# Performance work log

Hardware: AMD Instinct MI355X
Metric: run time of the kernel (lower is better)

## Reference

```python
import jax, jax.numpy as jnp
import numpy as np

WH, WW = 8, 8          # window height/width
NH = 8                 # num heads
DIM = 256              # channels
B_ = 512               # num_windows * batch
N = WH * WW            # tokens per window
HD = DIM // NH         # head dim


def _rel_constants():
    # log-spaced continuous relative coords table (Swin-V2 CPB input)
    ch = np.arange(-(WH - 1), WH, dtype=np.float32) / (WH - 1)
    cw = np.arange(-(WW - 1), WW, dtype=np.float32) / (WW - 1)
    table = np.stack(np.meshgrid(ch, cw, indexing='ij'), axis=-1)[None] * 8.0  # [1,2WH-1,2WW-1,2]
    table = np.sign(table) * np.log2(np.abs(table) + 1.0) / np.log2(8.0)
    # relative position index
    coords = np.stack(np.meshgrid(np.arange(WH), np.arange(WW), indexing='ij'))
    cf = coords.reshape(2, -1)
    rel = (cf[:, :, None] - cf[:, None, :]).transpose(1, 2, 0).astype(np.int64)
    rel[..., 0] += WH - 1
    rel[..., 1] += WW - 1
    rel[..., 0] *= 2 * WW - 1
    idx = rel.sum(-1)  # [N,N]
    return jnp.asarray(table, dtype=jnp.float32), jnp.asarray(idx)

TABLE, IDX = _rel_constants()


def setup_inputs() -> dict:
    key = jax.random.key(0)
    ks = jax.random.split(key, 16)
    s = lambda k, shape, sc=0.02: (jax.random.normal(k, shape, dtype=jnp.float32) * sc)
    inp = {
        'x1': jax.random.normal(ks[0], (B_, N, DIM), dtype=jnp.float32),
        'x2': jax.random.normal(ks[1], (B_, N, DIM), dtype=jnp.float32),
        'qkv_w1': s(ks[2], (3 * DIM, DIM)),
        'q_bias_1': jnp.zeros((DIM,), jnp.float32),
        'v_bias_1': jnp.zeros((DIM,), jnp.float32),
        'proj_w1': s(ks[3], (DIM, DIM)),
        'proj_b1': jnp.zeros((DIM,), jnp.float32),
        'logit_scale_1': jnp.log(10.0) * jnp.ones((NH, 1, 1), jnp.float32),
        'cpb1_w1': s(ks[4], (512, 2), 0.1),
        'cpb1_b1': jnp.zeros((512,), jnp.float32),
        'cpb1_w2': s(ks[5], (NH, 512), 0.1),
        'pc1_w': s(ks[6], (NH, 2 * NH), 0.1),
        'pc1_b': jnp.zeros((NH,), jnp.float32),
        'qkv_w2': s(ks[7], (3 * DIM, DIM)),
        'q_bias_2': jnp.zeros((DIM,), jnp.float32),
        'v_bias_2': jnp.zeros((DIM,), jnp.float32),
        'proj_w2': s(ks[8], (DIM, DIM)),
        'proj_b2': jnp.zeros((DIM,), jnp.float32),
        'logit_scale_2': jnp.log(10.0) * jnp.ones((NH, 1, 1), jnp.float32),
        'cpb2_w1': s(ks[9], (512, 2), 0.1),
        'cpb2_b1': jnp.zeros((512,), jnp.float32),
        'cpb2_w2': s(ks[10], (NH, 512), 0.1),
        'pc2_w': s(ks[11], (NH, 2 * NH), 0.1),
        'pc2_b': jnp.zeros((NH,), jnp.float32),
    }
    return inp


def _qkv(x, w, qb, vb):
    b = jnp.concatenate([qb, jnp.zeros_like(vb), vb])
    y = (x @ w.T + b).reshape(x.shape[0], N, 3, NH, HD).transpose(2, 0, 3, 1, 4)
    return y[0], y[1], y[2]  # each [B_, NH, N, HD]


def _l2norm(t):
    n = jnp.linalg.norm(t, axis=-1, keepdims=True)
    return t / jnp.maximum(n, 1e-12)


def _view(qn, k_same_n, k_diff_n, v, logit_scale, pc_w, pc_b, cw1, cb1, cw2, proj_w, proj_b):
    same = jnp.einsum('bhnd,bhmd->bhnm', qn, k_same_n)
    diff = jnp.einsum('bhnd,bhmd->bhnm', qn, k_diff_n)
    cat = jnp.concatenate([same, diff], axis=1).transpose(0, 2, 3, 1)  # [B,N,N,2H]
    scale = jnp.exp(jnp.minimum(logit_scale, jnp.log(100.0)))  # clamp at 1/0.01
    attn = (cat @ pc_w.T + pc_b).transpose(0, 3, 1, 2) * scale  # [B,H,N,N]
    # CPB MLP -> bias table -> gather
    tbl = (jax.nn.relu(TABLE @ cw1.T + cb1) @ cw2.T).reshape(-1, NH)  # [(2WH-1)*(2WW-1), H]
    bias = tbl[IDX.reshape(-1)].reshape(N, N, NH).transpose(2, 0, 1)  # [H,N,N]
    attn = attn + (16.0 * jax.nn.sigmoid(bias))[None]
    attn = jax.nn.softmax(attn, axis=-1)
    out = jnp.einsum('bhnm,bhmd->bhnd', attn, v).transpose(0, 2, 1, 3).reshape(-1, N, DIM)
    return out @ proj_w.T + proj_b


def reference(x1, x2, qkv_w1, q_bias_1, v_bias_1, proj_w1, proj_b1, logit_scale_1,
              cpb1_w1, cpb1_b1, cpb1_w2, pc1_w, pc1_b,
              qkv_w2, q_bias_2, v_bias_2, proj_w2, proj_b2, logit_scale_2,
              cpb2_w1, cpb2_b1, cpb2_w2, pc2_w, pc2_b):
    q1, k1, v1 = _qkv(x1, qkv_w1, q_bias_1, v_bias_1)
    q2, k2, v2 = _qkv(x2, qkv_w2, q_bias_2, v_bias_2)
    q1n, k1n = _l2norm(q1), _l2norm(k1)
    q2n, k2n = _l2norm(q2), _l2norm(k2)
    o1 = _view(q1n, k1n, k2n, v1, logit_scale_1, pc1_w, pc1_b, cpb1_w1, cpb1_b1, cpb1_w2, proj_w1, proj_b1)
    o2 = _view(q2n, k2n, k1n, v2, logit_scale_2, pc2_w, pc2_b, cpb2_w1, cpb2_b1, cpb2_w2, proj_w2, proj_b2)
    return o1, o2
```

## Files before the change

### kernel.cpp

```cpp
#include <hip/hip_runtime.h>

typedef _Float16 f16;
typedef f16  f16x8  __attribute__((ext_vector_type(8)));
typedef f16  f16x4v __attribute__((ext_vector_type(4)));
typedef f16  f16x2  __attribute__((ext_vector_type(2)));
typedef float f32x4 __attribute__((ext_vector_type(4)));

#define MFMA_F16(a,b,c) __builtin_amdgcn_mfma_f32_16x16x32_f16((a),(b),(c),0,0,0)

#define NWIN 512
#define SB_QST 3088
#define SB_KST 48
#define BUFX_ST 264
#define BUFO_HEAD 2304
#define VT_ST 72
#define SM_BYTES 70656
#define STBL_OFF 49408

__device__ __forceinline__ f16x8 ld_f16x8(const float* __restrict__ p) {
  f32x4 a = *(const f32x4*)p;
  f32x4 b = *(const f32x4*)(p + 4);
  f16x8 r;
  r[0] = (f16)a[0]; r[1] = (f16)a[1]; r[2] = (f16)a[2]; r[3] = (f16)a[3];
  r[4] = (f16)b[0]; r[5] = (f16)b[1]; r[6] = (f16)b[2]; r[7] = (f16)b[3];
  return r;
}

__global__ __launch_bounds__(256) void prep_all(
    const float* __restrict__ w1a, const float* __restrict__ b1a,
    const float* __restrict__ w2a,
    const float* __restrict__ w1b, const float* __restrict__ b1b,
    const float* __restrict__ w2b,
    const float* __restrict__ qkvw1, const float* __restrict__ qkvw2,
    const float* __restrict__ pw1, const float* __restrict__ pw2,
    float* __restrict__ sg16,
    f16* __restrict__ wq1f, f16* __restrict__ wq2f,
    f16* __restrict__ pw1f, f16* __restrict__ pw2f) {
  const int b = blockIdx.x;
  if (b >= 450) {
    const int cb = b - 450;
    const float* src; f16* dst; int base;
    if (cb < 96)       { src = qkvw1; dst = wq1f; base = cb * 2048; }
    else if (cb < 192) { src = qkvw2; dst = wq2f; base = (cb - 96) * 2048; }
    else if (cb < 224) { src = pw1;   dst = pw1f; base = (cb - 192) * 2048; }
    else               { src = pw2;   dst = pw2f; base = (cb - 224) * 2048; }
    const int o = base + threadIdx.x * 8;
    *(f16x8*)(dst + o) = ld_f16x8(src + o);
    return;
  }
  const int view = b / 225;
  const int e    = b % 225;
  const float* __restrict__ w1 = view ? w1b : w1a;
  const float* __restrict__ b1 = view ? b1b : b1a;
  const float* __restrict__ w2 = view ? w2b : w2a;
  const int t = threadIdx.x;
  const int i = e / 15, j = e % 15;
  const float vi = 8.0f * (float)(i - 7) * (1.0f / 7.0f);
  const float vj = 8.0f * (float)(j - 7) * (1.0f / 7.0f);
  const float in0 = copysignf(log2f(fabsf(vi) + 1.0f) * (1.0f / 3.0f), vi);
  const float in1 = copysignf(log2f(fabsf(vj) + 1.0f) * (1.0f / 3.0f), vj);
  float acc[8] = {0.f,0.f,0.f,0.f,0.f,0.f,0.f,0.f};
#pragma unroll
  for (int uu = 0; uu < 2; ++uu) {
    const int u = t + uu * 256;
    float hv = fmaxf(w1[2*u] * in0 + w1[2*u+1] * in1 + b1[u], 0.0f);
#pragma unroll
    for (int hh = 0; hh < 8; ++hh) acc[hh] += w2[hh*512 + u] * hv;
  }
#pragma unroll
  for (int off = 32; off >= 1; off >>= 1)
#pragma unroll
    for (int hh = 0; hh < 8; ++hh) acc[hh] += __shfl_xor(acc[hh], off, 64);
  __shared__ float red[4][8];
  if ((t & 63) == 0) {
#pragma unroll
    for (int hh = 0; hh < 8; ++hh) red[t >> 6][hh] = acc[hh];
  }
  __syncthreads();
  if (t < 8) {
    float s = red[0][t] + red[1][t] + red[2][t] + red[3][t];
    sg16[(view * 225 + e) * 8 + t] = 16.0f / (1.0f + __expf(-s));
  }
}

__global__ __launch_bounds__(512, 2) void fused_attn(
    const float* __restrict__ x1, const float* __restrict__ x2,
    const f16* __restrict__ qkvw1, const float* __restrict__ qb1, const float* __restrict__ vb1,
    const f16* __restrict__ qkvw2, const float* __restrict__ qb2, const float* __restrict__ vb2,
    const float* __restrict__ pcw1, const float* __restrict__ pcb1, const float* __restrict__ ls1,
    const float* __restrict__ pcw2, const float* __restrict__ pcb2, const float* __restrict__ ls2,
    const f16* __restrict__ pw1, const float* __restrict__ pb1,
    const f16* __restrict__ pw2, const float* __restrict__ pb2,
    const float* __restrict__ sg16,
    float* __restrict__ outp) {
  const int win = blockIdx.x;
  const int tid = threadIdx.x;
  const int lane = tid & 63, h = tid >> 6;
  const int quad = lane >> 4, m = lane & 15;

  __shared__ __align__(16) char sm[SM_BYTES];
  f16* bufX  = (f16*)sm;
  f16* bufO  = (f16*)(sm + 33792);
  char* Sbc  = sm;
  f16* preB  = (f16*)sm;
  float* sTbl = (float*)(sm + STBL_OFF);

  const f32x4 z4 = {0.f, 0.f, 0.f, 0.f};
  f16x8 aqF[2][4], kfF[2][4], bvF[2][2][2];
  f16* oh = bufO + h * BUFO_HEAD;

  for (int view = 0; view < 2; ++view) {
    const float* __restrict__ xv = (view ? x2 : x1) + (size_t)win * (64 * 256);
    const f16* __restrict__ W    = view ? qkvw2 : qkvw1;
    const float* __restrict__ qb = view ? qb2 : qb1;
    const float* __restrict__ vb = view ? vb2 : vb1;

    __syncthreads();
    for (int i = tid; i < 2048; i += 512) {
      const int row = i >> 5, c8 = i & 31;
      *(f16x8*)(bufX + row * BUFX_ST + c8 * 8) = ld_f16x8(xv + row * 256 + c8 * 8);
    }
    __syncthreads();

    for (int sec = 0; sec < 3; ++sec) {
      f32x4 acc0[4], acc1[4];
#pragma unroll
      for (int t = 0; t < 4; ++t) { acc0[t] = z4; acc1[t] = z4; }
      const f16* wb = W + (size_t)(sec * 256 + h * 32) * 256 + quad * 8;
#pragma unroll 2
      for (int k8 = 0; k8 < 8; ++k8) {
        f16x8 a0 = *(const f16x8*)(wb + (size_t)m * 256 + k8 * 32);
        f16x8 a1 = *(const f16x8*)(wb + (size_t)(16 + m) * 256 + k8 * 32);
#pragma unroll
        for (int tt = 0; tt < 4; ++tt) {
          f16x8 bfr = *(const f16x8*)(bufX + (tt * 16 + m) * BUFX_ST + k8 * 32 + quad * 8);
          acc0[tt] = MFMA_F16(a0, bfr, acc0[tt]);
          acc1[tt] = MFMA_F16(a1, bfr, acc1[tt]);
        }
      }
      float bs0[4], bs1[4];
#pragma unroll
      for (int r = 0; r < 4; ++r) {
        int c0 = h * 32 + quad * 4 + r;
        bs0[r] = (sec == 0) ? qb[c0] : (sec == 2 ? vb[c0] : 0.f);
        bs1[r] = (sec == 0) ? qb[c0 + 16] : (sec == 2 ? vb[c0 + 16] : 0.f);
      }
#pragma unroll
      for (int tt = 0; tt < 4; ++tt) {
        float v0[4], v1[4];
#pragma unroll
        for (int r = 0; r < 4; ++r) { v0[r] = acc0[tt][r] + bs0[r]; v1[r] = acc1[tt][r] + bs1[r]; }
        if (sec < 2) {
          float ss = 0.f;
#pragma unroll
          for (int r = 0; r < 4; ++r) ss += v0[r] * v0[r] + v1[r] * v1[r];
          ss += __shfl_xor(ss, 16, 64);
          ss += __shfl_xor(ss, 32, 64);
          float s = 1.0f / fmaxf(sqrtf(ss), 1e-12f);
#pragma unroll
          for (int r = 0; r < 4; ++r) { v0[r] *= s; v1[r] *= s; }
        }
        const int n = tt * 16 + m;
        if (sec < 2) {
          f16x4v p0, p1;
#pragma unroll
          for (int r = 0; r < 4; ++r) { p0[r] = (f16)v0[r]; p1[r] = (f16)v1[r]; }
          char* ob = (char*)oh;
          const int sw = (n & 7) << 4;
          *(f16x4v*)(ob + ((n * 64 + quad * 8) ^ sw))      = p0;
          *(f16x4v*)(ob + ((n * 64 + 32 + quad * 8) ^ sw)) = p1;
        } else {
#pragma unroll
          for (int r = 0; r < 4; ++r) {
            oh[(quad * 4 + r) * VT_ST + n]      = (f16)v0[r];
            oh[(quad * 4 + 16 + r) * VT_ST + n] = (f16)v1[r];
          }
        }
      }
      if (sec == 0) {
#pragma unroll
        for (int rt = 0; rt < 4; ++rt) {
          const int n = rt * 16 + m;
          aqF[view][rt] = *(const f16x8*)((char*)oh + ((n * 64 + quad * 16) ^ ((n & 7) << 4)));
        }
      } else if (sec == 1) {
#pragma unroll
        for (int ct = 0; ct < 4; ++ct) {
          const int n = ct * 16 + m;
          kfF[view][ct] = *(const f16x8*)((char*)oh + ((n * 64 + quad * 16) ^ ((n & 7) << 4)));
        }
      } else {
#pragma unroll
        for (int nt = 0; nt < 2; ++nt)
#pragma unroll
          for (int kv = 0; kv < 2; ++kv)
            bvF[view][nt][kv] = *(const f16x8*)(oh + (nt * 16 + m) * VT_ST + kv * 32 + quad * 8);
      }
    }
  }
  __syncthreads();

  for (int i = tid; i < 3600; i += 512) sTbl[i] = sg16[i];

#pragma unroll
  for (int view = 0; view < 2; ++view) {
    const float* __restrict__ pcw = view ? pcw2 : pcw1;
    float pcwf[16];
#pragma unroll
    for (int c = 0; c < 16; ++c) pcwf[c] = pcw[h * 16 + c];
    const float pcb_h = (view ? pcb2 : pcb1)[h];
    const float lsv = (view ? ls2 : ls1)[h];
    const float scale_h = __expf(fminf(lsv, 4.6051702f));
    const float pcbs = pcb_h * scale_h;
    const float* tblv = sTbl + view * 1800;

    f32x4 oacc[4][2];
#pragma unroll
    for (int rt = 0; rt < 4; ++rt) {
      f16x8 aq = aqF[view][rt];
      __builtin_amdgcn_s_setprio(1);
#pragma unroll
      for (int ct = 0; ct < 4; ++ct) {
        const int kk = ct * 16 + m;
        const int wbase = kk * SB_KST + (h << 2);
        f32x4 Ss = MFMA_F16(aq, kfF[view][ct], z4);
        f32x4 Sd = MFMA_F16(aq, kfF[1 - view][ct], z4);
#pragma unroll
        for (int r = 0; r < 4; ++r) {
          f16x2 pr; pr[0] = (f16)Ss[r]; pr[1] = (f16)Sd[r];
          *(f16x2*)(Sbc + (quad * 4 + r) * SB_QST + wbase) = pr;
        }
      }
      __builtin_amdgcn_s_setprio(0);
      __syncthreads();

      const int n = rt * 16 + m;
      const int nh_ = n >> 3, nw_ = n & 7;
      const int rbase = m * SB_QST;
      float logit[16];
#pragma unroll
      for (int j = 0; j < 16; ++j) {
        const int mm = (j < 8) ? (quad * 8 + j) : (32 + quad * 8 + (j - 8));
        const int b0 = rbase + mm * SB_KST;
        f16x8 s0 = *(const f16x8*)(Sbc + b0);
        f16x8 s1 = *(const f16x8*)(Sbc + b0 + 16);
        float mix = 0.f;
#pragma unroll
        for (int c = 0; c < 4; ++c) {
          mix += pcwf[c]      * (float)s0[2*c] + pcwf[8 + c]  * (float)s0[2*c+1];
          mix += pcwf[4 + c]  * (float)s1[2*c] + pcwf[12 + c] * (float)s1[2*c+1];
        }
        const int idx = (nh_ - (mm >> 3) + 7) * 15 + (nw_ - (mm & 7) + 7);
        logit[j] = mix * scale_h + pcbs + tblv[idx * 8 + h];
      }
      float mx = -1e30f;
#pragma unroll
      for (int j = 0; j < 16; ++j) mx = fmaxf(mx, logit[j]);
      mx = fmaxf(mx, __shfl_xor(mx, 16, 64));
      mx = fmaxf(mx, __shfl_xor(mx, 32, 64));
      float p[16], sum = 0.f;
#pragma unroll
      for (int j = 0; j < 16; ++j) { p[j] = __expf(logit[j] - mx); sum += p[j]; }
      sum += __shfl_xor(sum, 16, 64);
      sum += __shfl_xor(sum, 32, 64);
      float inv = 1.0f / sum;
      f16x8 av0, av1;
#pragma unroll
      for (int j = 0; j < 8; ++j) { av0[j] = (f16)(p[j] * inv); av1[j] = (f16)(p[8 + j] * inv); }
      __builtin_amdgcn_s_setprio(1);
#pragma unroll
      for (int nt = 0; nt < 2; ++nt) {
        f32x4 z = z4;
        z = MFMA_F16(av0, bvF[view][nt][0], z);
        z = MFMA_F16(av1, bvF[view][nt][1], z);
        oacc[rt][nt] = z;
      }
      __builtin_amdgcn_s_setprio(0);
      __syncthreads();
    }

#pragma unroll
    for (int mt = 0; mt < 4; ++mt)
#pragma unroll
      for (int nt = 0; nt < 2; ++nt)
#pragma unroll
        for (int r = 0; r < 4; ++r)
          preB[(mt * 16 + quad * 4 + r) * 264 + h * 32 + nt * 16 + m] = (f16)oacc[mt][nt][r];
    __syncthreads();

    const f16* __restrict__ Wp = view ? pw2 : pw1;
    const float* __restrict__ pb = view ? pb2 : pb1;
    f32x4 pacc0[4], pacc1[4];
#pragma unroll
    for (int t = 0; t < 4; ++t) { pacc0[t] = z4; pacc1[t] = z4; }
#pragma unroll 2
    for (int ks = 0; ks < 8; ++ks) {
      f16x8 pa0 = *(const f16x8*)(Wp + (size_t)(h * 32 + m) * 256 + ks * 32 + quad * 8);
      f16x8 pa1 = *(const f16x8*)(Wp + (size_t)(h * 32 + 16 + m) * 256 + ks * 32 + quad * 8);
#pragma unroll
      for (int tt = 0; tt < 4; ++tt) {
        f16x8 bfr = *(const f16x8*)(preB + (tt * 16 + m) * 264 + ks * 32 + quad * 8);
        pacc0[tt] = MFMA_F16(pa0, bfr, pacc0[tt]);
        pacc1[tt] = MFMA_F16(pa1, bfr, pacc1[tt]);
      }
    }
    float* obase = outp + (size_t)(view * NWIN + win) * (64 * 256);
#pragma unroll
    for (int tt = 0; tt < 4; ++tt) {
      f32x4 p0, p1;
#pragma unroll
      for (int r = 0; r < 4; ++r) {
        p0[r] = pacc0[tt][r] + pb[h * 32 + quad * 4 + r];
        p1[r] = pacc1[tt][r] + pb[h * 32 + 16 + quad * 4 + r];
      }
      const int n = tt * 16 + m;
      *(f32x4*)(obase + n * 256 + h * 32 + quad * 4)      = p0;
      *(f32x4*)(obase + n * 256 + h * 32 + 16 + quad * 4) = p1;
    }
    __syncthreads();
  }
}

extern "C" void kernel_launch(void* const* d_in, const int* in_sizes, int n_in,
                              void* d_out, int out_size, void* d_ws, size_t ws_size,
                              hipStream_t stream) {
  (void)in_sizes; (void)n_in; (void)out_size; (void)ws_size;
  const float* x1   = (const float*)d_in[0];
  const float* x2   = (const float*)d_in[1];
  const float* qkvw1= (const float*)d_in[2];
  const float* qb1  = (const float*)d_in[3];
  const float* vb1  = (const float*)d_in[4];
  const float* pw1  = (const float*)d_in[5];
  const float* pb1  = (const float*)d_in[6];
  const float* ls1  = (const float*)d_in[7];
  const float* cw11 = (const float*)d_in[8];
  const float* cb11 = (const float*)d_in[9];
  const float* cw12 = (const float*)d_in[10];
  const float* pcw1 = (const float*)d_in[11];
  const float* pcb1 = (const float*)d_in[12];
  const float* qkvw2= (const float*)d_in[13];
  const float* qb2  = (const float*)d_in[14];
  const float* vb2  = (const float*)d_in[15];
  const float* pw2  = (const float*)d_in[16];
  const float* pb2  = (const float*)d_in[17];
  const float* ls2  = (const float*)d_in[18];
  const float* cw21 = (const float*)d_in[19];
  const float* cb21 = (const float*)d_in[20];
  const float* cw22 = (const float*)d_in[21];
  const float* pcw2 = (const float*)d_in[22];
  const float* pcb2 = (const float*)d_in[23];

  float* SG16 = (float*)d_ws;
  f16* wq1f = (f16*)((char*)d_ws + 14400);
  f16* wq2f = wq1f + 196608;
  f16* pw1f = wq2f + 196608;
  f16* pw2f = pw1f + 65536;
  float* out = (float*)d_out;

  prep_all<<<706, 256, 0, stream>>>(cw11, cb11, cw12, cw21, cb21, cw22,
                                    qkvw1, qkvw2, pw1, pw2,
                                    SG16, wq1f, wq2f, pw1f, pw2f);
  fused_attn<<<NWIN, 512, 0, stream>>>(x1, x2,
      wq1f, qb1, vb1, wq2f, qb2, vb2,
      pcw1, pcb1, ls1, pcw2, pcb2, ls2,
      pw1f, pb1, pw2f, pb2, SG16, out);
}
```

Measured before the change: 293.0 us.

## Fold head-mixing into K blend and process both views concurrently per block

```diff
diff --git a/kernel.cpp b/kernel.cpp
--- a/kernel.cpp
+++ b/kernel.cpp
@@ -3,19 +3,24 @@
 typedef _Float16 f16;
 typedef f16  f16x8  __attribute__((ext_vector_type(8)));
 typedef f16  f16x4v __attribute__((ext_vector_type(4)));
-typedef f16  f16x2  __attribute__((ext_vector_type(2)));
 typedef float f32x4 __attribute__((ext_vector_type(4)));
 
 #define MFMA_F16(a,b,c) __builtin_amdgcn_mfma_f32_16x16x32_f16((a),(b),(c),0,0,0)
 
 #define NWIN 512
-#define SB_QST 3088
-#define SB_KST 48
-#define BUFX_ST 264
-#define BUFO_HEAD 2304
-#define VT_ST 72
-#define SM_BYTES 70656
-#define STBL_OFF 49408
+#define RA 0
+#define RB 32768
+#define RC 65536
+#define RD 98304
+#define RE 131072
+#define SM_BYTES 163840
+
+__device__ __forceinline__ int swz512(int row, int colByte) {
+  return row * 512 + (colByte ^ ((row & 7) << 4));
+}
+__device__ __forceinline__ int swz128(int row, int colByte) {
+  return row * 128 + (colByte ^ ((row & 7) << 4));
+}
 
 __device__ __forceinline__ f16x8 ld_f16x8(const float* __restrict__ p) {
   f32x4 a = *(const f32x4*)p;
@@ -33,7 +38,7 @@
     const float* __restrict__ w2b,
     const float* __restrict__ qkvw1, const float* __restrict__ qkvw2,
     const float* __restrict__ pw1, const float* __restrict__ pw2,
-    float* __restrict__ sg16,
+    float* __restrict__ tblT,
     f16* __restrict__ wq1f, f16* __restrict__ wq2f,
     f16* __restrict__ pw1f, f16* __restrict__ pw2f) {
   const int b = blockIdx.x;
@@ -79,11 +84,11 @@
   __syncthreads();
   if (t < 8) {
     float s = red[0][t] + red[1][t] + red[2][t] + red[3][t];
-    sg16[(view * 225 + e) * 8 + t] = 16.0f / (1.0f + __expf(-s));
-  }
-}
-
-__global__ __launch_bounds__(512, 2) void fused_attn(
+    tblT[(view * 8 + t) * 226 + e] = 16.0f / (1.0f + __expf(-s));
+  }
+}
+
+__global__ __launch_bounds__(1024, 4) void fused_attn(
     const float* __restrict__ x1, const float* __restrict__ x2,
     const f16* __restrict__ qkvw1, const float* __restrict__ qb1, const float* __restrict__ vb1,
     const f16* __restrict__ qkvw2, const float* __restrict__ qb2, const float* __restrict__ vb2,
@@ -91,53 +96,57 @@
     const float* __restrict__ pcw2, const float* __restrict__ pcb2, const float* __restrict__ ls2,
     const f16* __restrict__ pw1, const float* __restrict__ pb1,
     const f16* __restrict__ pw2, const float* __restrict__ pb2,
-    const float* __restrict__ sg16,
+    const float* __restrict__ tblT,
     float* __restrict__ outp) {
-  const int win = blockIdx.x;
   const int tid = threadIdx.x;
-  const int lane = tid & 63, h = tid >> 6;
+  const int lane = tid & 63;
+  const int w = tid >> 6;
   const int quad = lane >> 4, m = lane & 15;
+  const int vgrp = w >> 3;
+  const int h = w & 7;
 
   __shared__ __align__(16) char sm[SM_BYTES];
-  f16* bufX  = (f16*)sm;
-  f16* bufO  = (f16*)(sm + 33792);
-  char* Sbc  = sm;
-  f16* preB  = (f16*)sm;
-  float* sTbl = (float*)(sm + STBL_OFF);
-
   const f32x4 z4 = {0.f, 0.f, 0.f, 0.f};
-  f16x8 aqF[2][4], kfF[2][4], bvF[2][2][2];
-  f16* oh = bufO + h * BUFO_HEAD;
-
-  for (int view = 0; view < 2; ++view) {
-    const float* __restrict__ xv = (view ? x2 : x1) + (size_t)win * (64 * 256);
-    const f16* __restrict__ W    = view ? qkvw2 : qkvw1;
-    const float* __restrict__ qb = view ? qb2 : qb1;
-    const float* __restrict__ vb = view ? vb2 : vb1;
-
-    __syncthreads();
-    for (int i = tid; i < 2048; i += 512) {
-      const int row = i >> 5, c8 = i & 31;
-      *(f16x8*)(bufX + row * BUFX_ST + c8 * 8) = ld_f16x8(xv + row * 256 + c8 * 8);
+
+  f16x8 bvF[2][2][2];
+
+  char* bufX = sm + (vgrp ? RB : RA);
+  char* Karr = sm + (vgrp ? RD : RC);
+  const f16* W = vgrp ? qkvw2 : qkvw1;
+  const float* qb = vgrp ? qb2 : qb1;
+  const float* vb = vgrp ? vb2 : vb1;
+
+  for (int wi = 0; wi < 2; ++wi) {
+    const int win = blockIdx.x * 2 + wi;
+
+    for (int i = tid; i < 4096; i += 1024) {
+      const int vv = i >> 11, row = (i >> 5) & 63, c8 = i & 31;
+      const float* src = (vv ? x2 : x1) + (size_t)win * (64 * 256) + row * 256 + c8 * 8;
+      *(f16x8*)(sm + (vv ? RB : RA) + swz512(row, c8 * 16)) = ld_f16x8(src);
     }
     __syncthreads();
 
-    for (int sec = 0; sec < 3; ++sec) {
+    for (int si = 0; si < 3; ++si) {
+      const int sec = 2 - si;
       f32x4 acc0[4], acc1[4];
 #pragma unroll
       for (int t = 0; t < 4; ++t) { acc0[t] = z4; acc1[t] = z4; }
       const f16* wb = W + (size_t)(sec * 256 + h * 32) * 256 + quad * 8;
+      __builtin_amdgcn_s_setprio(1);
 #pragma unroll 2
       for (int k8 = 0; k8 < 8; ++k8) {
         f16x8 a0 = *(const f16x8*)(wb + (size_t)m * 256 + k8 * 32);
         f16x8 a1 = *(const f16x8*)(wb + (size_t)(16 + m) * 256 + k8 * 32);
 #pragma unroll
         for (int tt = 0; tt < 4; ++tt) {
-          f16x8 bfr = *(const f16x8*)(bufX + (tt * 16 + m) * BUFX_ST + k8 * 32 + quad * 8);
+          f16x8 bfr = *(const f16x8*)(bufX + swz512(tt * 16 + m, k8 * 64 + quad * 16));
           acc0[tt] = MFMA_F16(a0, bfr, acc0[tt]);
           acc1[tt] = MFMA_F16(a1, bfr, acc1[tt]);
         }
       }
+      __builtin_amdgcn_s_setprio(0);
+      if (sec == 0) __syncthreads();
+
       float bs0[4], bs1[4];
 #pragma unroll
       for (int r = 0; r < 4; ++r) {
@@ -156,166 +165,170 @@
           for (int r = 0; r < 4; ++r) ss += v0[r] * v0[r] + v1[r] * v1[r];
           ss += __shfl_xor(ss, 16, 64);
           ss += __shfl_xor(ss, 32, 64);
-          float s = 1.0f / fmaxf(sqrtf(ss), 1e-12f);
-#pragma unroll
-          for (int r = 0; r < 4; ++r) { v0[r] *= s; v1[r] *= s; }
+          float sc = 1.0f / fmaxf(sqrtf(ss), 1e-12f);
+#pragma unroll
+          for (int r = 0; r < 4; ++r) { v0[r] *= sc; v1[r] *= sc; }
         }
         const int n = tt * 16 + m;
         if (sec < 2) {
+          char* dst = (sec == 0) ? bufX : Karr;
           f16x4v p0, p1;
 #pragma unroll
           for (int r = 0; r < 4; ++r) { p0[r] = (f16)v0[r]; p1[r] = (f16)v1[r]; }
-          char* ob = (char*)oh;
-          const int sw = (n & 7) << 4;
-          *(f16x4v*)(ob + ((n * 64 + quad * 8) ^ sw))      = p0;
-          *(f16x4v*)(ob + ((n * 64 + 32 + quad * 8) ^ sw)) = p1;
+          *(f16x4v*)(dst + swz512(n, h * 64 + quad * 8))      = p0;
+          *(f16x4v*)(dst + swz512(n, h * 64 + 32 + quad * 8)) = p1;
         } else {
 #pragma unroll
           for (int r = 0; r < 4; ++r) {
-            oh[(quad * 4 + r) * VT_ST + n]      = (f16)v0[r];
-            oh[(quad * 4 + 16 + r) * VT_ST + n] = (f16)v1[r];
+            *(f16*)(Karr + h * 4096 + swz128(quad * 4 + r, n * 2))      = (f16)v0[r];
+            *(f16*)(Karr + h * 4096 + swz128(16 + quad * 4 + r, n * 2)) = (f16)v1[r];
           }
         }
       }
-      if (sec == 0) {
-#pragma unroll
-        for (int rt = 0; rt < 4; ++rt) {
-          const int n = rt * 16 + m;
-          aqF[view][rt] = *(const f16x8*)((char*)oh + ((n * 64 + quad * 16) ^ ((n & 7) << 4)));
-        }
-      } else if (sec == 1) {
-#pragma unroll
-        for (int ct = 0; ct < 4; ++ct) {
-          const int n = ct * 16 + m;
-          kfF[view][ct] = *(const f16x8*)((char*)oh + ((n * 64 + quad * 16) ^ ((n & 7) << 4)));
-        }
-      } else {
+      if (sec == 2) {
+        __syncthreads();
+#pragma unroll
+        for (int vv = 0; vv < 2; ++vv) {
+          char* vs = sm + (vv ? RD : RC) + h * 4096;
+#pragma unroll
+          for (int nt = 0; nt < 2; ++nt)
+#pragma unroll
+            for (int kv = 0; kv < 2; ++kv)
+              bvF[vv][nt][kv] = *(const f16x8*)(vs + swz128(nt * 16 + m, kv * 64 + quad * 16));
+        }
+        __syncthreads();
+      }
+    }
+    __syncthreads();
+
+    for (int vv = 0; vv < 2; ++vv) {
+      const float* pcw = vv ? pcw2 : pcw1;
+      f16 ws[8], wd[8];
+#pragma unroll
+      for (int c = 0; c < 8; ++c) {
+        ws[c] = (f16)pcw[h * 16 + c];
+        wd[c] = (f16)pcw[h * 16 + 8 + c];
+      }
+      const float pcb_h = (vv ? pcb2 : pcb1)[h];
+      const float lsv = (vv ? ls2 : ls1)[h];
+      const float scale_h = __expf(fminf(lsv, 4.6051702f));
+      const float pcbs = pcb_h * scale_h;
+      const float* tb = tblT + (vv * 8 + h) * 226;
+      char* Q  = sm + (vv ? RB : RA);
+      char* Ks = sm + (vv ? RD : RC);
+      char* Kd = sm + (vv ? RC : RD);
+
+      f32x4 acc[2][4];
+#pragma unroll
+      for (int a = 0; a < 2; ++a)
+#pragma unroll
+        for (int b = 0; b < 4; ++b) acc[a][b] = z4;
+      __builtin_amdgcn_s_setprio(1);
+#pragma unroll
+      for (int c = 0; c < 8; ++c) {
+        f16x8 qa0 = *(const f16x8*)(Q + swz512(vgrp * 32 + m,      c * 64 + quad * 16));
+        f16x8 qa1 = *(const f16x8*)(Q + swz512(vgrp * 32 + 16 + m, c * 64 + quad * 16));
+        const f16 wsc = ws[c], wdc = wd[c];
+#pragma unroll
+        for (int kt = 0; kt < 4; ++kt) {
+          f16x8 k1 = *(const f16x8*)(Ks + swz512(kt * 16 + m, c * 64 + quad * 16));
+          f16x8 k2 = *(const f16x8*)(Kd + swz512(kt * 16 + m, c * 64 + quad * 16));
+          f16x8 kk;
+#pragma unroll
+          for (int j = 0; j < 8; ++j) kk[j] = (f16)(k1[j] * wsc + k2[j] * wdc);
+          acc[0][kt] = MFMA_F16(qa0, kk, acc[0][kt]);
+          acc[1][kt] = MFMA_F16(qa1, kk, acc[1][kt]);
+        }
+      }
+      __builtin_amdgcn_s_setprio(0);
+
+      f32x4 oacc[2][2];
+      char* Pt = sm + RE + w * 2048;
+#pragma unroll
+      for (int qtl = 0; qtl < 2; ++qtl) {
+        float logit[4][4];
+#pragma unroll
+        for (int kt = 0; kt < 4; ++kt) {
+          const int k0 = kt * 16 + m;
+          const int kh = k0 >> 3, kw = k0 & 7;
+#pragma unroll
+          for (int r = 0; r < 4; ++r) {
+            const int q = (vgrp * 2 + qtl) * 16 + quad * 4 + r;
+            const int idx = ((q >> 3) - kh + 7) * 15 + ((q & 7) - kw + 7);
+            logit[kt][r] = acc[qtl][kt][r] * scale_h + pcbs + tb[idx];
+          }
+        }
+#pragma unroll
+        for (int r = 0; r < 4; ++r) {
+          float mr = fmaxf(fmaxf(logit[0][r], logit[1][r]),
+                           fmaxf(logit[2][r], logit[3][r]));
+          mr = fmaxf(mr, __shfl_xor(mr, 1, 64));
+          mr = fmaxf(mr, __shfl_xor(mr, 2, 64));
+          mr = fmaxf(mr, __shfl_xor(mr, 4, 64));
+          mr = fmaxf(mr, __shfl_xor(mr, 8, 64));
+          float p0 = __expf(logit[0][r] - mr), p1 = __expf(logit[1][r] - mr);
+          float p2 = __expf(logit[2][r] - mr), p3 = __expf(logit[3][r] - mr);
+          float sr = p0 + p1 + p2 + p3;
+          sr += __shfl_xor(sr, 1, 64);
+          sr += __shfl_xor(sr, 2, 64);
+          sr += __shfl_xor(sr, 4, 64);
+          sr += __shfl_xor(sr, 8, 64);
+          const float inv = 1.0f / sr;
+          logit[0][r] = p0 * inv; logit[1][r] = p1 * inv;
+          logit[2][r] = p2 * inv; logit[3][r] = p3 * inv;
+        }
+#pragma unroll
+        for (int kt = 0; kt < 4; ++kt)
+#pragma unroll
+          for (int r = 0; r < 4; ++r)
+            *(f16*)(Pt + (quad * 4 + r) * 128 + (kt * 16 + m) * 2) = (f16)logit[kt][r];
+        f16x8 av0 = *(const f16x8*)(Pt + m * 128 + quad * 16);
+        f16x8 av1 = *(const f16x8*)(Pt + m * 128 + 64 + quad * 16);
+#pragma unroll
+        for (int nt = 0; nt < 2; ++nt) {
+          f32x4 z = z4;
+          z = MFMA_F16(av0, bvF[vv][nt][0], z);
+          z = MFMA_F16(av1, bvF[vv][nt][1], z);
+          oacc[qtl][nt] = z;
+        }
+      }
+
+      __syncthreads();
+      char* preB = sm + RA;
+#pragma unroll
+      for (int qtl = 0; qtl < 2; ++qtl)
 #pragma unroll
         for (int nt = 0; nt < 2; ++nt)
 #pragma unroll
-          for (int kv = 0; kv < 2; ++kv)
-            bvF[view][nt][kv] = *(const f16x8*)(oh + (nt * 16 + m) * VT_ST + kv * 32 + quad * 8);
-      }
-    }
-  }
-  __syncthreads();
-
-  for (int i = tid; i < 3600; i += 512) sTbl[i] = sg16[i];
-
-#pragma unroll
-  for (int view = 0; view < 2; ++view) {
-    const float* __restrict__ pcw = view ? pcw2 : pcw1;
-    float pcwf[16];
-#pragma unroll
-    for (int c = 0; c < 16; ++c) pcwf[c] = pcw[h * 16 + c];
-    const float pcb_h = (view ? pcb2 : pcb1)[h];
-    const float lsv = (view ? ls2 : ls1)[h];
-    const float scale_h = __expf(fminf(lsv, 4.6051702f));
-    const float pcbs = pcb_h * scale_h;
-    const float* tblv = sTbl + view * 1800;
-
-    f32x4 oacc[4][2];
-#pragma unroll
-    for (int rt = 0; rt < 4; ++rt) {
-      f16x8 aq = aqF[view][rt];
+          for (int r = 0; r < 4; ++r) {
+            const int row = vgrp * 32 + qtl * 16 + quad * 4 + r;
+            *(f16*)(preB + swz512(row, (h * 32 + nt * 16 + m) * 2)) = (f16)oacc[qtl][nt][r];
+          }
+      __syncthreads();
+      const f16* Wp = vv ? pw2 : pw1;
+      const float* pb = vv ? pb2 : pb1;
+      f32x4 pacc[4];
+#pragma unroll
+      for (int t = 0; t < 4; ++t) pacc[t] = z4;
       __builtin_amdgcn_s_setprio(1);
-#pragma unroll
-      for (int ct = 0; ct < 4; ++ct) {
-        const int kk = ct * 16 + m;
-        const int wbase = kk * SB_KST + (h << 2);
-        f32x4 Ss = MFMA_F16(aq, kfF[view][ct], z4);
-        f32x4 Sd = MFMA_F16(aq, kfF[1 - view][ct], z4);
-#pragma unroll
-        for (int r = 0; r < 4; ++r) {
-          f16x2 pr; pr[0] = (f16)Ss[r]; pr[1] = (f16)Sd[r];
-          *(f16x2*)(Sbc + (quad * 4 + r) * SB_QST + wbase) = pr;
+#pragma unroll 2
+      for (int ks = 0; ks < 8; ++ks) {
+        f16x8 pa = *(const f16x8*)(Wp + (size_t)(w * 16 + m) * 256 + ks * 32 + quad * 8);
+#pragma unroll
+        for (int tt = 0; tt < 4; ++tt) {
+          f16x8 bfr = *(const f16x8*)(preB + swz512(tt * 16 + m, ks * 64 + quad * 16));
+          pacc[tt] = MFMA_F16(pa, bfr, pacc[tt]);
         }
       }
       __builtin_amdgcn_s_setprio(0);
-      __syncthreads();
-
-      const int n = rt * 16 + m;
-      const int nh_ = n >> 3, nw_ = n & 7;
-      const int rbase = m * SB_QST;
-      float logit[16];
-#pragma unroll
-      for (int j = 0; j < 16; ++j) {
-        const int mm = (j < 8) ? (quad * 8 + j) : (32 + quad * 8 + (j - 8));
-        const int b0 = rbase + mm * SB_KST;
-        f16x8 s0 = *(const f16x8*)(Sbc + b0);
-        f16x8 s1 = *(const f16x8*)(Sbc + b0 + 16);
-        float mix = 0.f;
-#pragma unroll
-        for (int c = 0; c < 4; ++c) {
-          mix += pcwf[c]      * (float)s0[2*c] + pcwf[8 + c]  * (float)s0[2*c+1];
-          mix += pcwf[4 + c]  * (float)s1[2*c] + pcwf[12 + c] * (float)s1[2*c+1];
-        }
-        const int idx = (nh_ - (mm >> 3) + 7) * 15 + (nw_ - (mm & 7) + 7);
-        logit[j] = mix * scale_h + pcbs + tblv[idx * 8 + h];
-      }
-      float mx = -1e30f;
-#pragma unroll
-      for (int j = 0; j < 16; ++j) mx = fmaxf(mx, logit[j]);
-      mx = fmaxf(mx, __shfl_xor(mx, 16, 64));
-      mx = fmaxf(mx, __shfl_xor(mx, 32, 64));
-      float p[16], sum = 0.f;
-#pragma unroll
-      for (int j = 0; j < 16; ++j) { p[j] = __expf(logit[j] - mx); sum += p[j]; }
-      sum += __shfl_xor(sum, 16, 64);
-      sum += __shfl_xor(sum, 32, 64);
-      float inv = 1.0f / sum;
-      f16x8 av0, av1;
-#pragma unroll
-      for (int j = 0; j < 8; ++j) { av0[j] = (f16)(p[j] * inv); av1[j] = (f16)(p[8 + j] * inv); }
-      __builtin_amdgcn_s_setprio(1);
-#pragma unroll
-      for (int nt = 0; nt < 2; ++nt) {
-        f32x4 z = z4;
-        z = MFMA_F16(av0, bvF[view][nt][0], z);
-        z = MFMA_F16(av1, bvF[view][nt][1], z);
-        oacc[rt][nt] = z;
-      }
-      __builtin_amdgcn_s_setprio(0);
-      __syncthreads();
-    }
-
-#pragma unroll
-    for (int mt = 0; mt < 4; ++mt)
-#pragma unroll
-      for (int nt = 0; nt < 2; ++nt)
-#pragma unroll
-        for (int r = 0; r < 4; ++r)
-          preB[(mt * 16 + quad * 4 + r) * 264 + h * 32 + nt * 16 + m] = (f16)oacc[mt][nt][r];
-    __syncthreads();
-
-    const f16* __restrict__ Wp = view ? pw2 : pw1;
-    const float* __restrict__ pb = view ? pb2 : pb1;
-    f32x4 pacc0[4], pacc1[4];
-#pragma unroll
-    for (int t = 0; t < 4; ++t) { pacc0[t] = z4; pacc1[t] = z4; }
-#pragma unroll 2
-    for (int ks = 0; ks < 8; ++ks) {
-      f16x8 pa0 = *(const f16x8*)(Wp + (size_t)(h * 32 + m) * 256 + ks * 32 + quad * 8);
-      f16x8 pa1 = *(const f16x8*)(Wp + (size_t)(h * 32 + 16 + m) * 256 + ks * 32 + quad * 8);
+      float* obase = outp + (size_t)(vv * NWIN + win) * (64 * 256);
 #pragma unroll
       for (int tt = 0; tt < 4; ++tt) {
-        f16x8 bfr = *(const f16x8*)(preB + (tt * 16 + m) * 264 + ks * 32 + quad * 8);
-        pacc0[tt] = MFMA_F16(pa0, bfr, pacc0[tt]);
-        pacc1[tt] = MFMA_F16(pa1, bfr, pacc1[tt]);
-      }
-    }
-    float* obase = outp + (size_t)(view * NWIN + win) * (64 * 256);
-#pragma unroll
-    for (int tt = 0; tt < 4; ++tt) {
-      f32x4 p0, p1;
-#pragma unroll
-      for (int r = 0; r < 4; ++r) {
-        p0[r] = pacc0[tt][r] + pb[h * 32 + quad * 4 + r];
-        p1[r] = pacc1[tt][r] + pb[h * 32 + 16 + quad * 4 + r];
-      }
-      const int n = tt * 16 + m;
-      *(f32x4*)(obase + n * 256 + h * 32 + quad * 4)      = p0;
-      *(f32x4*)(obase + n * 256 + h * 32 + 16 + quad * 4) = p1;
+        f32x4 p0;
+#pragma unroll
+        for (int r = 0; r < 4; ++r) p0[r] = pacc[tt][r] + pb[w * 16 + quad * 4 + r];
+        *(f32x4*)(obase + (tt * 16 + m) * 256 + w * 16 + quad * 4) = p0;
+      }
     }
     __syncthreads();
   }
@@ -350,8 +363,8 @@
   const float* pcw2 = (const float*)d_in[22];
   const float* pcb2 = (const float*)d_in[23];
 
-  float* SG16 = (float*)d_ws;
-  f16* wq1f = (f16*)((char*)d_ws + 14400);
+  float* TBLT = (float*)d_ws;
+  f16* wq1f = (f16*)((char*)d_ws + 14464);
   f16* wq2f = wq1f + 196608;
   f16* pw1f = wq2f + 196608;
   f16* pw2f = pw1f + 65536;
@@ -359,9 +372,9 @@
 
   prep_all<<<706, 256, 0, stream>>>(cw11, cb11, cw12, cw21, cb21, cw22,
                                     qkvw1, qkvw2, pw1, pw2,
-                                    SG16, wq1f, wq2f, pw1f, pw2f);
-  fused_attn<<<NWIN, 512, 0, stream>>>(x1, x2,
+                                    TBLT, wq1f, wq2f, pw1f, pw2f);
+  fused_attn<<<256, 1024, 0, stream>>>(x1, x2,
       wq1f, qb1, vb1, wq2f, qb2, vb2,
       pcw1, pcb1, ls1, pcw2, pcb2, ls2,
-      pw1f, pb1, pw2f, pb2, SG16, out);
-}
+      pw1f, pb1, pw2f, pb2, TBLT, out);
+}
```

New measurement: 343.3 us. 1.17x slower.
